# Performance work log

Measured on AMD Instinct MI355X. Metric: run time of the kernel, lower is better.

## Reference

```python
import jax, jax.numpy as jnp
import numpy as np

NDIR = 6      # build_tree.num_directions()
IDIM = 256
ODIM = 512
B, L, NCH = 8, 4096, 8192


def setup_inputs() -> dict:
    key = jax.random.key(0)
    ks = jax.random.split(key, 9)
    last = jax.random.normal(ks[0], (B, NCH, IDIM), dtype=jnp.float32)
    child_l = jax.random.randint(ks[1], (L,), 0, NCH, dtype=jnp.int32)
    child_r = jax.random.randint(ks[2], (L,), 0, NCH, dtype=jnp.int32)
    vec = jax.random.randint(ks[3], (B, L), 0, NCH, dtype=jnp.int32)
    drev = jax.random.randint(ks[4], (NCH,), 0, 2, dtype=jnp.int32)
    dmap = jax.random.randint(ks[5], (NCH,), 0, NDIR, dtype=jnp.int32)
    # merge FC params: ndir independent Linear(2*idim -> odim) + PReLU(init=relu_weight)
    scale = 1.0 / np.sqrt(2 * IDIM)
    W_merge = jax.random.uniform(ks[6], (NDIR, ODIM, 2 * IDIM), jnp.float32, -scale, scale)
    b_merge = jax.random.uniform(ks[7], (NDIR, ODIM), jnp.float32, -scale, scale)
    alpha_merge = jnp.full((NDIR,), 0.005, dtype=jnp.float32)  # PReLU weight (relu_weight)
    return {"last": last, "W_merge": W_merge, "b_merge": b_merge,
            "alpha_merge": alpha_merge, "child_l": child_l, "child_r": child_r,
            "vec": vec, "drev": drev, "dmap": dmap}


def reference(last, W_merge, b_merge, alpha_merge, child_l, child_r, vec, drev, dmap):
    # child gathers: [B, L, idim]
    lch = last[:, child_l]
    rch = last[:, child_r]
    # per-element direction-reverse blending
    d = drev[vec][:, :, None].astype(last.dtype)          # [B, L, 1]
    a = lch * (1.0 - d) + rch * d
    b = rch * (1.0 - d) + lch * d
    ans = jnp.concatenate([a, b], axis=-1)                # [B, L, 2*idim]
    # routed merge: compute all ndir linears, then select per element (ndir is small)
    y_all = jnp.einsum('bli,doi->bldo', ans, W_merge) + b_merge   # [B, L, ndir, odim]
    dir_idx = dmap[vec]                                   # [B, L] in [0, ndir)
    y = jnp.take_along_axis(y_all, dir_idx[:, :, None, None], axis=2)[:, :, 0]  # [B, L, odim]
    alpha = alpha_merge[dir_idx][:, :, None]              # per-element PReLU slope
    return jnp.where(y > 0, y, alpha * y)
```

## Files before the change

### kernel.cpp

```cpp
#include <hip/hip_runtime.h>
#include <hip/hip_bf16.h>

#define BB 8
#define LL 4096
#define NCH 8192
#define IDIM 256
#define KDIM 512
#define ODIM 512
#define NDIR 6
#define TOT (BB * LL)

typedef short short8 __attribute__((ext_vector_type(8)));
typedef float floatx4 __attribute__((ext_vector_type(4)));

#define WS_LAST_OFF (64 + 2 * TOT)
#define LAST_ELEMS (BB * NCH * IDIM)
#define W_ELEMS (NDIR * ODIM * KDIM)
#define N_LAST8 (LAST_ELEMS / 8)
#define N_W8 (W_ELEMS / 8)

__device__ inline void async_copy16(const void* g, void* l) {
  __builtin_amdgcn_global_load_lds(
      (const __attribute__((address_space(1))) void*)g,
      (__attribute__((address_space(3))) void*)l, 16, 0, 0);
}

__device__ inline void cvt8(const float* __restrict__ src,
                            __hip_bfloat16* __restrict__ dst, int i) {
  const floatx4* s = (const floatx4*)src;
  floatx4 a = s[2 * i];
  floatx4 b = s[2 * i + 1];
  union { short8 v; __hip_bfloat16 h[8]; } u;
  u.h[0] = __float2bfloat16(a[0]); u.h[1] = __float2bfloat16(a[1]);
  u.h[2] = __float2bfloat16(a[2]); u.h[3] = __float2bfloat16(a[3]);
  u.h[4] = __float2bfloat16(b[0]); u.h[5] = __float2bfloat16(b[1]);
  u.h[6] = __float2bfloat16(b[2]); u.h[7] = __float2bfloat16(b[3]);
  ((short8*)dst)[i] = u.v;
}

__global__ __launch_bounds__(256) void prep_kernel(
    const float* __restrict__ last, const float* __restrict__ W,
    const int* __restrict__ vec, const int* __restrict__ dmap,
    int* __restrict__ ws) {
  __hip_bfloat16* last_bf = (__hip_bfloat16*)(ws + WS_LAST_OFF);
  __hip_bfloat16* W_bf = last_bf + LAST_ELEMS;
  int gid = blockIdx.x * 256 + threadIdx.x;
  if (gid < N_LAST8) {
    cvt8(last, last_bf, gid);
  } else if (gid < N_LAST8 + N_W8) {
    cvt8(W, W_bf, gid - N_LAST8);
  } else {
    __shared__ int lcnt[8];
    int tid = threadIdx.x;
    if (tid < 8) lcnt[tid] = 0;
    __syncthreads();
    int lin = gid - (N_LAST8 + N_W8);
    int dir = dmap[vec[lin]] & 7;
    atomicAdd(&lcnt[dir], 1);
    __syncthreads();
    if (tid < 8 && lcnt[tid]) atomicAdd(&ws[tid], lcnt[tid]);
  }
}

__global__ void scan_kernel(int* __restrict__ ws) {
  if (threadIdx.x == 0) {
    int s = 0;
    for (int d = 0; d < 8; ++d) { ws[16 + d] = s; s += ws[d]; }
  }
}

__global__ __launch_bounds__(256) void scatter_kernel(
    const int* __restrict__ vec, const int* __restrict__ child_l,
    const int* __restrict__ child_r, const int* __restrict__ drev,
    const int* __restrict__ dmap, int* __restrict__ ws) {
  __shared__ int lcnt[8];
  __shared__ int gbase[8];
  int* fill = ws + 8;
  const int* base = ws + 16;
  int* idx = ws + 64;
  int* rows = ws + 64 + TOT;

  int tid = threadIdx.x;
  if (tid < 8) lcnt[tid] = 0;
  __syncthreads();

  int lin = blockIdx.x * 256 + tid;
  int l = lin & (LL - 1);
  int v = vec[lin];
  int dir = dmap[v] & 7;
  int sw = drev[v];
  int cl = child_l[l];
  int cr = child_r[l];
  int r0 = sw ? cr : cl;
  int r1 = sw ? cl : cr;
  int pos = atomicAdd(&lcnt[dir], 1);
  __syncthreads();
  if (tid < 8) gbase[tid] = lcnt[tid] ? atomicAdd(&fill[tid], lcnt[tid]) : 0;
  __syncthreads();
  int slot = base[dir] + gbase[dir] + pos;
  idx[slot] = lin;
  rows[slot] = r0 | (r1 << 16);
}

__global__ __launch_bounds__(256) void gemm_kernel(
    const float* __restrict__ bias, const float* __restrict__ alpha_m,
    const int* __restrict__ ws, float* __restrict__ out) {
  __shared__ __hip_bfloat16 Als[128 * 64];
  __shared__ __hip_bfloat16 Bls[128 * 64];

  const int mt = blockIdx.y;
  const int nt = blockIdx.x;
  int d = -1, count = 0, off = 0, m_base = 0;
  {
    int tb = 0;
    for (int dd = 0; dd < NDIR; ++dd) {
      int c = ws[dd];
      int ntile = (c + 127) >> 7;
      if (mt < tb + ntile) { d = dd; count = c; off = ws[16 + dd]; m_base = (mt - tb) * 128; break; }
      tb += ntile;
    }
  }
  if (d < 0) return;

  const int* idx = ws + 64;
  const int* rows = ws + 64 + TOT;
  const __hip_bfloat16* last_bf = (const __hip_bfloat16*)(ws + WS_LAST_OFF);
  const __hip_bfloat16* W_bf = last_bf + LAST_ELEMS;

  const int tid = threadIdx.x;
  const int wave = __builtin_amdgcn_readfirstlane(tid >> 6);
  const int lane = tid & 63;
  const int lane15 = lane & 15;
  const int quad = lane >> 4;
  const int wm = wave >> 1;
  const int wn = wave & 1;
  const int n_blk = nt * 128;

  const __hip_bfloat16* ap0[4];
  const __hip_bfloat16* ap1[4];
  const __hip_bfloat16* bp[4];
  int ldsrow[4];
#pragma unroll
  for (int i = 0; i < 4; ++i) {
    int sr = wave * 32 + i * 8 + (lane >> 3);
    ldsrow[i] = (wave * 32 + i * 8) * 64;
    int lr = m_base + sr;
    if (lr >= count) lr = count - 1;
    int lin = idx[off + lr] & (TOT - 1);
    int rr = rows[off + lr];
    int b = lin >> 12;
    int r0 = rr & (NCH - 1);
    int r1 = (rr >> 16) & (NCH - 1);
    int xu = ((lane & 7) ^ (sr & 7)) * 8;
    ap0[i] = last_bf + (long long)(b * NCH + r0) * IDIM + xu;
    ap1[i] = last_bf + (long long)(b * NCH + r1) * IDIM + xu;
    int xuB = xu;
    bp[i] = W_bf + (long long)(d * ODIM + n_blk + sr) * KDIM + xuB;
  }

  floatx4 acc[4][4] = {};
  const int lx = lane15 & 7;

#pragma unroll
  for (int kt = 0; kt < 8; ++kt) {
    __syncthreads();
    const int ko = (kt & 3) * 64;
#pragma unroll
    for (int i = 0; i < 4; ++i) {
      const __hip_bfloat16* ga = (kt < 4 ? ap0[i] : ap1[i]) + ko;
      async_copy16(ga, &Als[ldsrow[i]]);
    }
#pragma unroll
    for (int i = 0; i < 4; ++i) {
      async_copy16(bp[i] + kt * 64, &Bls[ldsrow[i]]);
    }
    __syncthreads();

#pragma unroll
    for (int s = 0; s < 2; ++s) {
      const int xcol = ((quad + 4 * s) ^ lx) * 8;
      short8 a[4], b[4];
#pragma unroll
      for (int i = 0; i < 4; ++i)
        a[i] = *(const short8*)&Als[(wm * 64 + i * 16 + lane15) * 64 + xcol];
#pragma unroll
      for (int j = 0; j < 4; ++j)
        b[j] = *(const short8*)&Bls[(wn * 64 + j * 16 + lane15) * 64 + xcol];
#pragma unroll
      for (int i = 0; i < 4; ++i)
#pragma unroll
        for (int j = 0; j < 4; ++j)
          acc[i][j] = __builtin_amdgcn_mfma_f32_16x16x32_bf16(a[i], b[j], acc[i][j], 0, 0, 0);
    }
  }

  const float alpha = alpha_m[d];
  float bj[4];
#pragma unroll
  for (int j = 0; j < 4; ++j)
    bj[j] = bias[d * ODIM + n_blk + wn * 64 + j * 16 + lane15];

#pragma unroll
  for (int i = 0; i < 4; ++i) {
#pragma unroll
    for (int reg = 0; reg < 4; ++reg) {
      int row_id = m_base + wm * 64 + i * 16 + quad * 4 + reg;
      if (row_id >= count) continue;
      int lin = idx[off + row_id] & (TOT - 1);
      float* orow = out + (long long)lin * ODIM + n_blk + wn * 64;
#pragma unroll
      for (int j = 0; j < 4; ++j) {
        float y = acc[i][j][reg] + bj[j];
        y = y > 0.f ? y : alpha * y;
        orow[j * 16 + lane15] = y;
      }
    }
  }
}

extern "C" void kernel_launch(void* const* d_in, const int* in_sizes, int n_in,
                              void* d_out, int out_size, void* d_ws, size_t ws_size,
                              hipStream_t stream) {
  const float* last = (const float*)d_in[0];
  const float* W = (const float*)d_in[1];
  const float* bias = (const float*)d_in[2];
  const float* alpha = (const float*)d_in[3];
  const int* child_l = (const int*)d_in[4];
  const int* child_r = (const int*)d_in[5];
  const int* vec = (const int*)d_in[6];
  const int* drev = (const int*)d_in[7];
  const int* dmap = (const int*)d_in[8];

  int* ws = (int*)d_ws;

  hipMemsetAsync(ws, 0, 64 * sizeof(int), stream);
  int prep_blocks = (N_LAST8 + N_W8 + TOT) / 256;
  prep_kernel<<<prep_blocks, 256, 0, stream>>>(last, W, vec, dmap, ws);
  scan_kernel<<<1, 64, 0, stream>>>(ws);
  scatter_kernel<<<TOT / 256, 256, 0, stream>>>(vec, child_l, child_r, drev, dmap, ws);
  dim3 grid(ODIM / 128, TOT / 128 + NDIR, 1);
  gemm_kernel<<<grid, 256, 0, stream>>>(bias, alpha, ws, (float*)d_out);
}
```

Measured before the change: 168.5 us.

## Fuse fp32-to-bf16 conversion of gathered rows into GEMM, drop LDS staging

```diff
diff --git a/kernel.cpp b/kernel.cpp
--- a/kernel.cpp
+++ b/kernel.cpp
@@ -13,17 +13,12 @@
 typedef short short8 __attribute__((ext_vector_type(8)));
 typedef float floatx4 __attribute__((ext_vector_type(4)));
 
-#define WS_LAST_OFF (64 + 2 * TOT)
-#define LAST_ELEMS (BB * NCH * IDIM)
+#define WS_W_OFF (64 + 2 * TOT)
 #define W_ELEMS (NDIR * ODIM * KDIM)
-#define N_LAST8 (LAST_ELEMS / 8)
 #define N_W8 (W_ELEMS / 8)
 
-__device__ inline void async_copy16(const void* g, void* l) {
-  __builtin_amdgcn_global_load_lds(
-      (const __attribute__((address_space(1))) void*)g,
-      (__attribute__((address_space(3))) void*)l, 16, 0, 0);
-}
+#define GEMM_NWG 1048
+#define GEMM_CHUNK 131
 
 __device__ inline void cvt8(const float* __restrict__ src,
                             __hip_bfloat16* __restrict__ dst, int i) {
@@ -39,33 +34,22 @@
 }
 
 __global__ __launch_bounds__(256) void prep_kernel(
-    const float* __restrict__ last, const float* __restrict__ W,
-    const int* __restrict__ vec, const int* __restrict__ dmap,
-    int* __restrict__ ws) {
-  __hip_bfloat16* last_bf = (__hip_bfloat16*)(ws + WS_LAST_OFF);
-  __hip_bfloat16* W_bf = last_bf + LAST_ELEMS;
+    const float* __restrict__ W, const int* __restrict__ vec,
+    const int* __restrict__ dmap, int* __restrict__ ws) {
+  __hip_bfloat16* W_bf = (__hip_bfloat16*)(ws + WS_W_OFF);
   int gid = blockIdx.x * 256 + threadIdx.x;
-  if (gid < N_LAST8) {
-    cvt8(last, last_bf, gid);
-  } else if (gid < N_LAST8 + N_W8) {
-    cvt8(W, W_bf, gid - N_LAST8);
+  if (gid < N_W8) {
+    cvt8(W, W_bf, gid);
   } else {
     __shared__ int lcnt[8];
     int tid = threadIdx.x;
     if (tid < 8) lcnt[tid] = 0;
     __syncthreads();
-    int lin = gid - (N_LAST8 + N_W8);
+    int lin = gid - N_W8;
     int dir = dmap[vec[lin]] & 7;
     atomicAdd(&lcnt[dir], 1);
     __syncthreads();
     if (tid < 8 && lcnt[tid]) atomicAdd(&ws[tid], lcnt[tid]);
-  }
-}
-
-__global__ void scan_kernel(int* __restrict__ ws) {
-  if (threadIdx.x == 0) {
-    int s = 0;
-    for (int d = 0; d < 8; ++d) { ws[16 + d] = s; s += ws[d]; }
   }
 }
 
@@ -75,13 +59,18 @@
     const int* __restrict__ dmap, int* __restrict__ ws) {
   __shared__ int lcnt[8];
   __shared__ int gbase[8];
+  __shared__ int baseS[8];
   int* fill = ws + 8;
-  const int* base = ws + 16;
   int* idx = ws + 64;
   int* rows = ws + 64 + TOT;
 
   int tid = threadIdx.x;
-  if (tid < 8) lcnt[tid] = 0;
+  if (tid < 8) {
+    lcnt[tid] = 0;
+    int s = 0;
+    for (int i = 0; i < tid; ++i) s += ws[i];
+    baseS[tid] = s;
+  }
   __syncthreads();
 
   int lin = blockIdx.x * 256 + tid;
@@ -97,35 +86,36 @@
   __syncthreads();
   if (tid < 8) gbase[tid] = lcnt[tid] ? atomicAdd(&fill[tid], lcnt[tid]) : 0;
   __syncthreads();
-  int slot = base[dir] + gbase[dir] + pos;
+  int slot = baseS[dir] + gbase[dir] + pos;
   idx[slot] = lin;
   rows[slot] = r0 | (r1 << 16);
 }
 
-__global__ __launch_bounds__(256) void gemm_kernel(
-    const float* __restrict__ bias, const float* __restrict__ alpha_m,
-    const int* __restrict__ ws, float* __restrict__ out) {
-  __shared__ __hip_bfloat16 Als[128 * 64];
-  __shared__ __hip_bfloat16 Bls[128 * 64];
-
-  const int mt = blockIdx.y;
-  const int nt = blockIdx.x;
+__global__ __launch_bounds__(256, 2) void gemm_kernel(
+    const float* __restrict__ last, const float* __restrict__ bias,
+    const float* __restrict__ alpha_m, const int* __restrict__ ws,
+    float* __restrict__ out) {
+  int flat = blockIdx.y * 4 + blockIdx.x;
+  int swz = (flat & 7) * GEMM_CHUNK + (flat >> 3);
+  const int mt = swz >> 2;
+  const int nt = swz & 3;
+
   int d = -1, count = 0, off = 0, m_base = 0;
   {
-    int tb = 0;
+    int tb = 0, run = 0;
     for (int dd = 0; dd < NDIR; ++dd) {
       int c = ws[dd];
       int ntile = (c + 127) >> 7;
-      if (mt < tb + ntile) { d = dd; count = c; off = ws[16 + dd]; m_base = (mt - tb) * 128; break; }
-      tb += ntile;
+      if (mt < tb + ntile) { d = dd; count = c; off = run; m_base = (mt - tb) * 128; break; }
+      tb += ntile; run += c;
     }
   }
   if (d < 0) return;
 
   const int* idx = ws + 64;
   const int* rows = ws + 64 + TOT;
-  const __hip_bfloat16* last_bf = (const __hip_bfloat16*)(ws + WS_LAST_OFF);
-  const __hip_bfloat16* W_bf = last_bf + LAST_ELEMS;
+  const char* W_bf = (const char*)(ws + WS_W_OFF);
+  const char* lastc = (const char*)last;
 
   const int tid = threadIdx.x;
   const int wave = __builtin_amdgcn_readfirstlane(tid >> 6);
@@ -136,62 +126,71 @@
   const int wn = wave & 1;
   const int n_blk = nt * 128;
 
-  const __hip_bfloat16* ap0[4];
-  const __hip_bfloat16* ap1[4];
-  const __hip_bfloat16* bp[4];
-  int ldsrow[4];
+  int aoff0[4], aoff1[4];
 #pragma unroll
   for (int i = 0; i < 4; ++i) {
-    int sr = wave * 32 + i * 8 + (lane >> 3);
-    ldsrow[i] = (wave * 32 + i * 8) * 64;
-    int lr = m_base + sr;
+    int lr = m_base + wm * 64 + i * 16 + lane15;
     if (lr >= count) lr = count - 1;
     int lin = idx[off + lr] & (TOT - 1);
     int rr = rows[off + lr];
     int b = lin >> 12;
-    int r0 = rr & (NCH - 1);
-    int r1 = (rr >> 16) & (NCH - 1);
-    int xu = ((lane & 7) ^ (sr & 7)) * 8;
-    ap0[i] = last_bf + (long long)(b * NCH + r0) * IDIM + xu;
-    ap1[i] = last_bf + (long long)(b * NCH + r1) * IDIM + xu;
-    int xuB = xu;
-    bp[i] = W_bf + (long long)(d * ODIM + n_blk + sr) * KDIM + xuB;
-  }
+    aoff0[i] = ((b * NCH + (rr & (NCH - 1))) * IDIM + quad * 8) * 4;
+    aoff1[i] = ((b * NCH + ((rr >> 16) & (NCH - 1))) * IDIM + quad * 8) * 4;
+  }
+  int boff[4];
+#pragma unroll
+  for (int j = 0; j < 4; ++j)
+    boff[j] = ((d * ODIM + n_blk + wn * 64 + j * 16 + lane15) * KDIM + quad * 8) * 2;
 
   floatx4 acc[4][4] = {};
-  const int lx = lane15 & 7;
-
-#pragma unroll
-  for (int kt = 0; kt < 8; ++kt) {
-    __syncthreads();
-    const int ko = (kt & 3) * 64;
+  floatx4 pA[2][4][2];
+  short8 pB[2][4];
+
+#pragma unroll
+  for (int i = 0; i < 4; ++i) {
+    const char* p = lastc + aoff0[i];
+    pA[0][i][0] = *(const floatx4*)p;
+    pA[0][i][1] = *(const floatx4*)(p + 16);
+  }
+#pragma unroll
+  for (int j = 0; j < 4; ++j)
+    pB[0][j] = *(const short8*)(W_bf + boff[j]);
+
+#pragma unroll
+  for (int t = 0; t < 16; ++t) {
+    const int cur = t & 1, nxt = cur ^ 1;
+    if (t < 15) {
+      const int tn = t + 1;
+      const int half = tn >> 3;
+      const int cA = (((tn >> 1) & 3) * 64 + (tn & 1) * 32) * 4;
+#pragma unroll
+      for (int i = 0; i < 4; ++i) {
+        const char* p = lastc + (half ? aoff1[i] : aoff0[i]) + cA;
+        pA[nxt][i][0] = *(const floatx4*)p;
+        pA[nxt][i][1] = *(const floatx4*)(p + 16);
+      }
+      const int cB = tn * 32 * 2;
+#pragma unroll
+      for (int j = 0; j < 4; ++j)
+        pB[nxt][j] = *(const short8*)(W_bf + boff[j] + cB);
+    }
+    short8 a[4];
 #pragma unroll
     for (int i = 0; i < 4; ++i) {
-      const __hip_bfloat16* ga = (kt < 4 ? ap0[i] : ap1[i]) + ko;
-      async_copy16(ga, &Als[ldsrow[i]]);
-    }
-#pragma unroll
-    for (int i = 0; i < 4; ++i) {
-      async_copy16(bp[i] + kt * 64, &Bls[ldsrow[i]]);
-    }
-    __syncthreads();
-
-#pragma unroll
-    for (int s = 0; s < 2; ++s) {
-      const int xcol = ((quad + 4 * s) ^ lx) * 8;
-      short8 a[4], b[4];
-#pragma unroll
-      for (int i = 0; i < 4; ++i)
-        a[i] = *(const short8*)&Als[(wm * 64 + i * 16 + lane15) * 64 + xcol];
+      const floatx4 lo = pA[cur][i][0];
+      const floatx4 hi = pA[cur][i][1];
+      union { short8 v; __hip_bfloat16 h[8]; } u;
+      u.h[0] = __float2bfloat16(lo[0]); u.h[1] = __float2bfloat16(lo[1]);
+      u.h[2] = __float2bfloat16(lo[2]); u.h[3] = __float2bfloat16(lo[3]);
+      u.h[4] = __float2bfloat16(hi[0]); u.h[5] = __float2bfloat16(hi[1]);
+      u.h[6] = __float2bfloat16(hi[2]); u.h[7] = __float2bfloat16(hi[3]);
+      a[i] = u.v;
+    }
+#pragma unroll
+    for (int i = 0; i < 4; ++i)
 #pragma unroll
       for (int j = 0; j < 4; ++j)
-        b[j] = *(const short8*)&Bls[(wn * 64 + j * 16 + lane15) * 64 + xcol];
-#pragma unroll
-      for (int i = 0; i < 4; ++i)
-#pragma unroll
-        for (int j = 0; j < 4; ++j)
-          acc[i][j] = __builtin_amdgcn_mfma_f32_16x16x32_bf16(a[i], b[j], acc[i][j], 0, 0, 0);
-    }
+        acc[i][j] = __builtin_amdgcn_mfma_f32_16x16x32_bf16(a[i], pB[cur][j], acc[i][j], 0, 0, 0);
   }
 
   const float alpha = alpha_m[d];
@@ -234,10 +233,8 @@
   int* ws = (int*)d_ws;
 
   hipMemsetAsync(ws, 0, 64 * sizeof(int), stream);
-  int prep_blocks = (N_LAST8 + N_W8 + TOT) / 256;
-  prep_kernel<<<prep_blocks, 256, 0, stream>>>(last, W, vec, dmap, ws);
-  scan_kernel<<<1, 64, 0, stream>>>(ws);
+  prep_kernel<<<(N_W8 + TOT) / 256, 256, 0, stream>>>(W, vec, dmap, ws);
   scatter_kernel<<<TOT / 256, 256, 0, stream>>>(vec, child_l, child_r, drev, dmap, ws);
   dim3 grid(ODIM / 128, TOT / 128 + NDIR, 1);
-  gemm_kernel<<<grid, 256, 0, stream>>>(bias, alpha, ws, (float*)d_out);
-}
+  gemm_kernel<<<grid, 256, 0, stream>>>(last, bias, alpha, ws, (float*)d_out);
+}
```

After: 255.6 us. 1.52x slower.

## Double-buffer A tiles, load W fragments directly, swizzle blocks, drop scan kernel

Applied to the files above, without the earlier changes.

```diff
diff --git a/kernel.cpp b/kernel.cpp
--- a/kernel.cpp
+++ b/kernel.cpp
@@ -18,6 +18,8 @@
 #define W_ELEMS (NDIR * ODIM * KDIM)
 #define N_LAST8 (LAST_ELEMS / 8)
 #define N_W8 (W_ELEMS / 8)
+
+#define GEMM_CHUNK 131
 
 __device__ inline void async_copy16(const void* g, void* l) {
   __builtin_amdgcn_global_load_lds(
@@ -62,26 +64,24 @@
   }
 }
 
-__global__ void scan_kernel(int* __restrict__ ws) {
-  if (threadIdx.x == 0) {
-    int s = 0;
-    for (int d = 0; d < 8; ++d) { ws[16 + d] = s; s += ws[d]; }
-  }
-}
-
 __global__ __launch_bounds__(256) void scatter_kernel(
     const int* __restrict__ vec, const int* __restrict__ child_l,
     const int* __restrict__ child_r, const int* __restrict__ drev,
     const int* __restrict__ dmap, int* __restrict__ ws) {
   __shared__ int lcnt[8];
   __shared__ int gbase[8];
+  __shared__ int baseS[8];
   int* fill = ws + 8;
-  const int* base = ws + 16;
   int* idx = ws + 64;
   int* rows = ws + 64 + TOT;
 
   int tid = threadIdx.x;
-  if (tid < 8) lcnt[tid] = 0;
+  if (tid < 8) {
+    lcnt[tid] = 0;
+    int s = 0;
+    for (int i = 0; i < tid; ++i) s += ws[i];
+    baseS[tid] = s;
+  }
   __syncthreads();
 
   int lin = blockIdx.x * 256 + tid;
@@ -97,7 +97,7 @@
   __syncthreads();
   if (tid < 8) gbase[tid] = lcnt[tid] ? atomicAdd(&fill[tid], lcnt[tid]) : 0;
   __syncthreads();
-  int slot = base[dir] + gbase[dir] + pos;
+  int slot = baseS[dir] + gbase[dir] + pos;
   idx[slot] = lin;
   rows[slot] = r0 | (r1 << 16);
 }
@@ -105,19 +105,21 @@
 __global__ __launch_bounds__(256) void gemm_kernel(
     const float* __restrict__ bias, const float* __restrict__ alpha_m,
     const int* __restrict__ ws, float* __restrict__ out) {
-  __shared__ __hip_bfloat16 Als[128 * 64];
-  __shared__ __hip_bfloat16 Bls[128 * 64];
-
-  const int mt = blockIdx.y;
-  const int nt = blockIdx.x;
+  __shared__ __hip_bfloat16 Als[2][128 * 64];
+
+  int flat = blockIdx.y * 4 + blockIdx.x;
+  int swz = (flat & 7) * GEMM_CHUNK + (flat >> 3);
+  const int mt = swz >> 2;
+  const int nt = swz & 3;
+
   int d = -1, count = 0, off = 0, m_base = 0;
   {
-    int tb = 0;
+    int tb = 0, run = 0;
     for (int dd = 0; dd < NDIR; ++dd) {
       int c = ws[dd];
       int ntile = (c + 127) >> 7;
-      if (mt < tb + ntile) { d = dd; count = c; off = ws[16 + dd]; m_base = (mt - tb) * 128; break; }
-      tb += ntile;
+      if (mt < tb + ntile) { d = dd; count = c; off = run; m_base = (mt - tb) * 128; break; }
+      tb += ntile; run += c;
     }
   }
   if (d < 0) return;
@@ -138,7 +140,6 @@
 
   const __hip_bfloat16* ap0[4];
   const __hip_bfloat16* ap1[4];
-  const __hip_bfloat16* bp[4];
   int ldsrow[4];
 #pragma unroll
   for (int i = 0; i < 4; ++i) {
@@ -154,44 +155,53 @@
     int xu = ((lane & 7) ^ (sr & 7)) * 8;
     ap0[i] = last_bf + (long long)(b * NCH + r0) * IDIM + xu;
     ap1[i] = last_bf + (long long)(b * NCH + r1) * IDIM + xu;
-    int xuB = xu;
-    bp[i] = W_bf + (long long)(d * ODIM + n_blk + sr) * KDIM + xuB;
-  }
+  }
+  const __hip_bfloat16* bp[4];
+#pragma unroll
+  for (int j = 0; j < 4; ++j)
+    bp[j] = W_bf + (long long)(d * ODIM + n_blk + wn * 64 + j * 16 + lane15) * KDIM + quad * 8;
 
   floatx4 acc[4][4] = {};
   const int lx = lane15 & 7;
 
 #pragma unroll
+  for (int i = 0; i < 4; ++i) async_copy16(ap0[i], &Als[0][ldsrow[i]]);
+  __syncthreads();
+
+#pragma unroll
   for (int kt = 0; kt < 8; ++kt) {
-    __syncthreads();
-    const int ko = (kt & 3) * 64;
-#pragma unroll
-    for (int i = 0; i < 4; ++i) {
-      const __hip_bfloat16* ga = (kt < 4 ? ap0[i] : ap1[i]) + ko;
-      async_copy16(ga, &Als[ldsrow[i]]);
-    }
-#pragma unroll
-    for (int i = 0; i < 4; ++i) {
-      async_copy16(bp[i] + kt * 64, &Bls[ldsrow[i]]);
-    }
-    __syncthreads();
+    const int cur = kt & 1;
+    short8 bfr[2][4];
+#pragma unroll
+    for (int s = 0; s < 2; ++s)
+#pragma unroll
+      for (int j = 0; j < 4; ++j)
+        bfr[s][j] = *(const short8*)(bp[j] + kt * 64 + s * 32);
+
+    if (kt < 7) {
+      const int tn = kt + 1;
+      const int ko = (tn & 3) * 64;
+#pragma unroll
+      for (int i = 0; i < 4; ++i) {
+        const __hip_bfloat16* ga = (tn < 4 ? ap0[i] : ap1[i]) + ko;
+        async_copy16(ga, &Als[cur ^ 1][ldsrow[i]]);
+      }
+    }
 
 #pragma unroll
     for (int s = 0; s < 2; ++s) {
       const int xcol = ((quad + 4 * s) ^ lx) * 8;
-      short8 a[4], b[4];
+      short8 a[4];
 #pragma unroll
       for (int i = 0; i < 4; ++i)
-        a[i] = *(const short8*)&Als[(wm * 64 + i * 16 + lane15) * 64 + xcol];
-#pragma unroll
-      for (int j = 0; j < 4; ++j)
-        b[j] = *(const short8*)&Bls[(wn * 64 + j * 16 + lane15) * 64 + xcol];
+        a[i] = *(const short8*)&Als[cur][(wm * 64 + i * 16 + lane15) * 64 + xcol];
 #pragma unroll
       for (int i = 0; i < 4; ++i)
 #pragma unroll
         for (int j = 0; j < 4; ++j)
-          acc[i][j] = __builtin_amdgcn_mfma_f32_16x16x32_bf16(a[i], b[j], acc[i][j], 0, 0, 0);
-    }
+          acc[i][j] = __builtin_amdgcn_mfma_f32_16x16x32_bf16(a[i], bfr[s][j], acc[i][j], 0, 0, 0);
+    }
+    __syncthreads();
   }
 
   const float alpha = alpha_m[d];
@@ -236,7 +246,6 @@
   hipMemsetAsync(ws, 0, 64 * sizeof(int), stream);
   int prep_blocks = (N_LAST8 + N_W8 + TOT) / 256;
   prep_kernel<<<prep_blocks, 256, 0, stream>>>(last, W, vec, dmap, ws);
-  scan_kernel<<<1, 64, 0, stream>>>(ws);
   scatter_kernel<<<TOT / 256, 256, 0, stream>>>(vec, child_l, child_r, drev, dmap, ws);
   dim3 grid(ODIM / 128, TOT / 128 + NDIR, 1);
   gemm_kernel<<<grid, 256, 0, stream>>>(bias, alpha, ws, (float*)d_out);
```

New measurement: 184.2 us. 1.09x slower.

## Fuse scatter into prep kernel and software-pipeline GEMM loads with multi-buffered LDS

Applied to the files above, without the earlier changes.

```diff
diff --git a/kernel.cpp b/kernel.cpp
--- a/kernel.cpp
+++ b/kernel.cpp
@@ -10,14 +10,19 @@
 #define NDIR 6
 #define TOT (BB * LL)
 
-typedef short short8 __attribute__((ext_vector_type(8)));
-typedef float floatx4 __attribute__((ext_vector_type(4)));
-
-#define WS_LAST_OFF (64 + 2 * TOT)
+#define CAP 8192
+#define IDX_OFF 64
+#define ROWS_OFF (64 + 8 * CAP)
+#define WS_LAST_OFF (64 + 16 * CAP)
 #define LAST_ELEMS (BB * NCH * IDIM)
 #define W_ELEMS (NDIR * ODIM * KDIM)
 #define N_LAST8 (LAST_ELEMS / 8)
 #define N_W8 (W_ELEMS / 8)
+
+#define GEMM_CHUNK 131
+
+typedef short short8 __attribute__((ext_vector_type(8)));
+typedef float floatx4 __attribute__((ext_vector_type(4)));
 
 __device__ inline void async_copy16(const void* g, void* l) {
   __builtin_amdgcn_global_load_lds(
@@ -40,8 +45,9 @@
 
 __global__ __launch_bounds__(256) void prep_kernel(
     const float* __restrict__ last, const float* __restrict__ W,
-    const int* __restrict__ vec, const int* __restrict__ dmap,
-    int* __restrict__ ws) {
+    const int* __restrict__ vec, const int* __restrict__ child_l,
+    const int* __restrict__ child_r, const int* __restrict__ drev,
+    const int* __restrict__ dmap, int* __restrict__ ws) {
   __hip_bfloat16* last_bf = (__hip_bfloat16*)(ws + WS_LAST_OFF);
   __hip_bfloat16* W_bf = last_bf + LAST_ELEMS;
   int gid = blockIdx.x * 256 + threadIdx.x;
@@ -51,79 +57,54 @@
     cvt8(W, W_bf, gid - N_LAST8);
   } else {
     __shared__ int lcnt[8];
+    __shared__ int gbase[8];
     int tid = threadIdx.x;
     if (tid < 8) lcnt[tid] = 0;
     __syncthreads();
     int lin = gid - (N_LAST8 + N_W8);
-    int dir = dmap[vec[lin]] & 7;
-    atomicAdd(&lcnt[dir], 1);
+    int l = lin & (LL - 1);
+    int v = vec[lin];
+    int dir = dmap[v] & 7;
+    int sw = drev[v];
+    int cl = child_l[l];
+    int cr = child_r[l];
+    int r0 = sw ? cr : cl;
+    int r1 = sw ? cl : cr;
+    int pos = atomicAdd(&lcnt[dir], 1);
     __syncthreads();
-    if (tid < 8 && lcnt[tid]) atomicAdd(&ws[tid], lcnt[tid]);
-  }
-}
-
-__global__ void scan_kernel(int* __restrict__ ws) {
-  if (threadIdx.x == 0) {
-    int s = 0;
-    for (int d = 0; d < 8; ++d) { ws[16 + d] = s; s += ws[d]; }
-  }
-}
-
-__global__ __launch_bounds__(256) void scatter_kernel(
-    const int* __restrict__ vec, const int* __restrict__ child_l,
-    const int* __restrict__ child_r, const int* __restrict__ drev,
-    const int* __restrict__ dmap, int* __restrict__ ws) {
-  __shared__ int lcnt[8];
-  __shared__ int gbase[8];
-  int* fill = ws + 8;
-  const int* base = ws + 16;
-  int* idx = ws + 64;
-  int* rows = ws + 64 + TOT;
-
-  int tid = threadIdx.x;
-  if (tid < 8) lcnt[tid] = 0;
-  __syncthreads();
-
-  int lin = blockIdx.x * 256 + tid;
-  int l = lin & (LL - 1);
-  int v = vec[lin];
-  int dir = dmap[v] & 7;
-  int sw = drev[v];
-  int cl = child_l[l];
-  int cr = child_r[l];
-  int r0 = sw ? cr : cl;
-  int r1 = sw ? cl : cr;
-  int pos = atomicAdd(&lcnt[dir], 1);
-  __syncthreads();
-  if (tid < 8) gbase[tid] = lcnt[tid] ? atomicAdd(&fill[tid], lcnt[tid]) : 0;
-  __syncthreads();
-  int slot = base[dir] + gbase[dir] + pos;
-  idx[slot] = lin;
-  rows[slot] = r0 | (r1 << 16);
+    if (tid < 8) gbase[tid] = lcnt[tid] ? atomicAdd(&ws[tid], lcnt[tid]) : 0;
+    __syncthreads();
+    int slot = dir * CAP + gbase[dir] + pos;
+    ws[IDX_OFF + slot] = lin;
+    ws[ROWS_OFF + slot] = r0 | (r1 << 16);
+  }
 }
 
 __global__ __launch_bounds__(256) void gemm_kernel(
     const float* __restrict__ bias, const float* __restrict__ alpha_m,
     const int* __restrict__ ws, float* __restrict__ out) {
-  __shared__ __hip_bfloat16 Als[128 * 64];
-  __shared__ __hip_bfloat16 Bls[128 * 64];
-
-  const int mt = blockIdx.y;
-  const int nt = blockIdx.x;
-  int d = -1, count = 0, off = 0, m_base = 0;
+  __shared__ __hip_bfloat16 Als[3][128 * 64];
+  __shared__ __hip_bfloat16 Bls[2][128 * 64];
+
+  int flat = blockIdx.y * 4 + blockIdx.x;
+  int swz = (flat & 7) * GEMM_CHUNK + (flat >> 3);
+  const int mt = swz >> 2;
+  const int nt = swz & 3;
+
+  int d = -1, count = 0, m_base = 0;
   {
     int tb = 0;
-    for (int dd = 0; dd < NDIR; ++dd) {
+    for (int dd = 0; dd < 8; ++dd) {
       int c = ws[dd];
       int ntile = (c + 127) >> 7;
-      if (mt < tb + ntile) { d = dd; count = c; off = ws[16 + dd]; m_base = (mt - tb) * 128; break; }
+      if (mt < tb + ntile) { d = dd; count = c; m_base = (mt - tb) * 128; break; }
       tb += ntile;
     }
   }
   if (d < 0) return;
 
-  const int* idx = ws + 64;
-  const int* rows = ws + 64 + TOT;
+  const int* idxA = ws + IDX_OFF + d * CAP;
+  const int* rowsA = ws + ROWS_OFF + d * CAP;
   const __hip_bfloat16* last_bf = (const __hip_bfloat16*)(ws + WS_LAST_OFF);
   const __hip_bfloat16* W_bf = last_bf + LAST_ELEMS;
 
@@ -146,46 +127,64 @@
     ldsrow[i] = (wave * 32 + i * 8) * 64;
     int lr = m_base + sr;
     if (lr >= count) lr = count - 1;
-    int lin = idx[off + lr] & (TOT - 1);
-    int rr = rows[off + lr];
+    int lin = idxA[lr] & (TOT - 1);
+    int rr = rowsA[lr];
     int b = lin >> 12;
     int r0 = rr & (NCH - 1);
     int r1 = (rr >> 16) & (NCH - 1);
     int xu = ((lane & 7) ^ (sr & 7)) * 8;
     ap0[i] = last_bf + (long long)(b * NCH + r0) * IDIM + xu;
     ap1[i] = last_bf + (long long)(b * NCH + r1) * IDIM + xu;
-    int xuB = xu;
-    bp[i] = W_bf + (long long)(d * ODIM + n_blk + sr) * KDIM + xuB;
+    bp[i] = W_bf + (long long)(d * ODIM + n_blk + sr) * KDIM + xu;
+  }
+
+#define STAGE_A(c, buf)                                              \
+  {                                                                  \
+    const int ko = ((c) & 3) * 64;                                   \
+    _Pragma("unroll") for (int i = 0; i < 4; ++i)                    \
+        async_copy16(((c) < 4 ? ap0[i] : ap1[i]) + ko,               \
+                     &Als[(buf)][ldsrow[i]]);                        \
+  }
+#define STAGE_B(c, buf)                                              \
+  {                                                                  \
+    _Pragma("unroll") for (int i = 0; i < 4; ++i)                    \
+        async_copy16(bp[i] + (c) * 64, &Bls[(buf)][ldsrow[i]]);      \
   }
 
   floatx4 acc[4][4] = {};
   const int lx = lane15 & 7;
 
-#pragma unroll
-  for (int kt = 0; kt < 8; ++kt) {
-    __syncthreads();
-    const int ko = (kt & 3) * 64;
-#pragma unroll
-    for (int i = 0; i < 4; ++i) {
-      const __hip_bfloat16* ga = (kt < 4 ? ap0[i] : ap1[i]) + ko;
-      async_copy16(ga, &Als[ldsrow[i]]);
-    }
-#pragma unroll
-    for (int i = 0; i < 4; ++i) {
-      async_copy16(bp[i] + kt * 64, &Bls[ldsrow[i]]);
-    }
-    __syncthreads();
-
+  STAGE_B(0, 0);
+  STAGE_A(0, 0);
+  STAGE_A(1, 1);
+
+#pragma unroll
+  for (int c = 0; c < 8; ++c) {
+    __builtin_amdgcn_s_barrier();
+    if (c < 7) STAGE_B(c + 1, (c + 1) & 1);
+    if (c < 6) STAGE_A(c + 2, (c + 2) % 3);
+    if (c < 6) {
+      asm volatile("s_waitcnt vmcnt(12)" ::: "memory");
+    } else if (c == 6) {
+      asm volatile("s_waitcnt vmcnt(8)" ::: "memory");
+    } else {
+      asm volatile("s_waitcnt vmcnt(0)" ::: "memory");
+    }
+    __builtin_amdgcn_sched_barrier(0);
+    __builtin_amdgcn_s_barrier();
+
+    const __hip_bfloat16* Ab = Als[c % 3];
+    const __hip_bfloat16* Bb = Bls[c & 1];
 #pragma unroll
     for (int s = 0; s < 2; ++s) {
       const int xcol = ((quad + 4 * s) ^ lx) * 8;
       short8 a[4], b[4];
 #pragma unroll
       for (int i = 0; i < 4; ++i)
-        a[i] = *(const short8*)&Als[(wm * 64 + i * 16 + lane15) * 64 + xcol];
+        a[i] = *(const short8*)&Ab[(wm * 64 + i * 16 + lane15) * 64 + xcol];
 #pragma unroll
       for (int j = 0; j < 4; ++j)
-        b[j] = *(const short8*)&Bls[(wn * 64 + j * 16 + lane15) * 64 + xcol];
+        b[j] = *(const short8*)&Bb[(wn * 64 + j * 16 + lane15) * 64 + xcol];
 #pragma unroll
       for (int i = 0; i < 4; ++i)
 #pragma unroll
@@ -206,7 +205,7 @@
     for (int reg = 0; reg < 4; ++reg) {
       int row_id = m_base + wm * 64 + i * 16 + quad * 4 + reg;
       if (row_id >= count) continue;
-      int lin = idx[off + row_id] & (TOT - 1);
+      int lin = idxA[row_id] & (TOT - 1);
       float* orow = out + (long long)lin * ODIM + n_blk + wn * 64;
 #pragma unroll
       for (int j = 0; j < 4; ++j) {
@@ -234,10 +233,9 @@
   int* ws = (int*)d_ws;
 
   hipMemsetAsync(ws, 0, 64 * sizeof(int), stream);
-  int prep_blocks = (N_LAST8 + N_W8 + TOT) / 256;
-  prep_kernel<<<prep_blocks, 256, 0, stream>>>(last, W, vec, dmap, ws);
-  scan_kernel<<<1, 64, 0, stream>>>(ws);
-  scatter_kernel<<<TOT / 256, 256, 0, stream>>>(vec, child_l, child_r, drev, dmap, ws);
+  int prep_blocks = N_LAST8 / 256 + N_W8 / 256 + TOT / 256;
+  prep_kernel<<<prep_blocks, 256, 0, stream>>>(last, W, vec, child_l, child_r,
+                                               drev, dmap, ws);
   dim3 grid(ODIM / 128, TOT / 128 + NDIR, 1);
   gemm_kernel<<<grid, 256, 0, stream>>>(bias, alpha, ws, (float*)d_out);
 }
```

After: 164.0 us. 1.03x faster.
